# Kernel optimization log

Hardware: AMD Instinct MI355X
Metric: run time of the kernel (lower is better)

Reference implementation:

```python
import jax, jax.numpy as jnp
import numpy as np

N_CON = 100000
NUM_VAR = 100000
E = 1250000
H = 64


def setup_inputs() -> dict:
    key = jax.random.key(0)
    ks = jax.random.split(key, 6)
    x_con = jax.random.normal(ks[0], (N_CON, H), dtype=jnp.float32)
    src = jax.random.randint(ks[1], (E,), 0, N_CON, dtype=jnp.int32)
    dst = jax.random.randint(ks[2], (E,), 0, NUM_VAR, dtype=jnp.int32)
    W = jax.random.normal(ks[3], (H, H), dtype=jnp.float32) * (1.0 / np.sqrt(H))
    b = jax.random.normal(ks[4], (H,), dtype=jnp.float32) * 0.02
    gamma = jnp.ones((H,), dtype=jnp.float32)
    beta = jnp.zeros((H,), dtype=jnp.float32)
    return {"x_con": x_con, "src": src, "dst": dst, "num_var": NUM_VAR,
            "W": W, "b": b, "gamma": gamma, "beta": beta}


def reference(x_con, src, dst, num_var, W, b, gamma, beta):
    # gather -> linear: (E, H)
    msg = x_con[src] @ W.T + b
    # degree (bincount) and degree-normalized scatter-add
    deg = jnp.zeros((num_var,), dtype=msg.dtype).at[dst].add(1.0)
    agg = jnp.zeros((num_var, msg.shape[1]), dtype=msg.dtype).at[dst].add(msg)
    agg = agg / (deg[:, None] + 1e-6)
    h = jax.nn.relu(agg)
    # LayerNorm (eps=1e-5, affine)
    mu = jnp.mean(h, axis=-1, keepdims=True)
    var = jnp.mean((h - mu) ** 2, axis=-1, keepdims=True)
    return (h - mu) * jax.lax.rsqrt(var + 1e-5) * gamma + beta
```

## Files before the change

kernel.cpp:

```cpp
#include <hip/hip_runtime.h>
#include <math.h>

#define HDIM 64
#define VPB 64
#define NBR 1600
#define MAXCAP 1072
#define PKSHIFT 25
#define PKMASK 0x1FFFFFF
#define SSTR 36

typedef __attribute__((ext_vector_type(8))) short s8v;
typedef __attribute__((ext_vector_type(4))) float f4v;

__device__ __forceinline__ int pkbf(float lo, float hi) {
    unsigned ul = __float_as_uint(lo) + 0x8000u;
    unsigned uh = __float_as_uint(hi) + 0x8000u;
    return (int)((ul >> 16) | (uh & 0xffff0000u));
}

__global__ __launch_bounds__(1024) void k_partition(
        const int* __restrict__ src, const int* __restrict__ dst,
        int* __restrict__ pairs, int* __restrict__ bcur,
        int E, int NB, int CAP) {
    __shared__ int hist[NBR], cur[NBR], gb[NBR];
    int t = threadIdx.x;
    int e0 = blockIdx.x << 12;

    for (int j = t; j < NBR; j += 1024) { hist[j] = 0; cur[j] = 0; }
    __syncthreads();

    int pk[4], bb[4];
    #pragma unroll
    for (int k = 0; k < 4; ++k) {
        int e = e0 + (k << 10) + t;
        pk[k] = -1; bb[k] = 0;
        if (e < E) {
            int d = dst[e];
            bb[k] = d >> 6;
            pk[k] = ((d & (VPB - 1)) << PKSHIFT) | src[e];
            atomicAdd(&hist[bb[k]], 1);
        }
    }
    __syncthreads();
    for (int j = t; j < NB; j += 1024) {
        int h = hist[j];
        if (h) gb[j] = j * CAP + atomicAdd(&bcur[j << 4], h);
    }
    __syncthreads();
    #pragma unroll
    for (int k = 0; k < 4; ++k) {
        if (pk[k] != -1) {
            int b = bb[k];
            int r = atomicAdd(&cur[b], 1);
            int g = gb[b] + r;
            if (g < (b + 1) * CAP) pairs[g] = pk[k];
        }
    }
}

__global__ __launch_bounds__(256, 4) void k_fused(
        const float* __restrict__ x, const int* __restrict__ pairs,
        const int* __restrict__ bcur, const float* __restrict__ W,
        const float* __restrict__ b, const float* __restrict__ gamma,
        const float* __restrict__ beta, float* __restrict__ out,
        int V, int CAP) {
    __shared__ int pbuf[MAXCAP];
    __shared__ int sidx[MAXCAP];
    __shared__ int vcnt[VPB], vcur[VPB], voff[VPB];
    __shared__ int sums[4 * 16 * SSTR];
    int t = threadIdx.x;
    int blk = blockIdx.x;
    int base = blk * CAP;
    int cnt = bcur[blk << 4]; if (cnt > CAP) cnt = CAP;

    if (t < VPB) vcnt[t] = 0;
    __syncthreads();
    for (int e = t; e < cnt; e += 256) {
        int pk = pairs[base + e];
        pbuf[e] = pk;
        atomicAdd(&vcnt[((unsigned)pk) >> PKSHIFT], 1);
    }
    __syncthreads();
    if (t < 64) {
        int c0 = vcnt[t];
        int pre = c0;
        #pragma unroll
        for (int off = 1; off < 64; off <<= 1) {
            int u = __shfl_up(pre, off, 64);
            if (t >= off) pre += u;
        }
        voff[t] = pre - c0;
        vcur[t] = pre - c0;
    }
    __syncthreads();
    for (int e = t; e < cnt; e += 256) {
        int pk = pbuf[e];
        int slot = atomicAdd(&vcur[((unsigned)pk) >> PKSHIFT], 1);
        sidx[slot] = pk & PKMASK;
    }
    __syncthreads();

    int wv = t >> 6, lane = t & 63, q = lane >> 4, c = lane & 15;
    int sbase = wv * (16 * SSTR);

    for (int j = 0; j < 8; ++j) {
        int lv0 = j << 1, lv1 = lv0 + 1;
        int vl0 = (wv << 4) + lv0, vl1 = vl0 + 1;
        int start0 = voff[vl0], dg0 = vcnt[vl0];
        int start1 = voff[vl1], dg1 = vcnt[vl1];

        float a0x = 0, a0y = 0, a0z = 0, a0w = 0;
        float a1x = 0, a1y = 0, a1z = 0, a1w = 0;
        int n = dg0 > dg1 ? dg0 : dg1;
        for (int t0 = 0; t0 < n; t0 += 16) {
            #pragma unroll
            for (int k = 0; k < 4; ++k) {
                int ii = t0 + (k << 2) + q;
                if (ii < dg0) {
                    int s = sidx[start0 + ii];
                    const float4 xv = *(const float4*)(x + ((size_t)s << 6) + (c << 2));
                    a0x += xv.x; a0y += xv.y; a0z += xv.z; a0w += xv.w;
                }
                if (ii < dg1) {
                    int s = sidx[start1 + ii];
                    const float4 xv = *(const float4*)(x + ((size_t)s << 6) + (c << 2));
                    a1x += xv.x; a1y += xv.y; a1z += xv.z; a1w += xv.w;
                }
            }
        }
        a0x += __shfl_xor(a0x, 16, 64); a1x += __shfl_xor(a1x, 16, 64);
        a0y += __shfl_xor(a0y, 16, 64); a1y += __shfl_xor(a1y, 16, 64);
        a0z += __shfl_xor(a0z, 16, 64); a1z += __shfl_xor(a1z, 16, 64);
        a0w += __shfl_xor(a0w, 16, 64); a1w += __shfl_xor(a1w, 16, 64);
        a0x += __shfl_xor(a0x, 32, 64); a1x += __shfl_xor(a1x, 32, 64);
        a0y += __shfl_xor(a0y, 32, 64); a1y += __shfl_xor(a1y, 32, 64);
        a0z += __shfl_xor(a0z, 32, 64); a1z += __shfl_xor(a1z, 32, 64);
        a0w += __shfl_xor(a0w, 32, 64); a1w += __shfl_xor(a1w, 32, 64);

        if (q == 0) {
            int o0 = sbase + lv0 * SSTR + (c << 1);
            sums[o0]     = pkbf(a0x, a0y);
            sums[o0 + 1] = pkbf(a0z, a0w);
            int o1 = sbase + lv1 * SSTR + (c << 1);
            sums[o1]     = pkbf(a1x, a1y);
            sums[o1 + 1] = pkbf(a1z, a1w);
        }
    }
    __builtin_amdgcn_wave_barrier();

    union { int i4[4]; s8v v; } af[4][2];
    #pragma unroll
    for (int i = 0; i < 4; ++i)
        #pragma unroll
        for (int hh = 0; hh < 2; ++hh) {
            const float* wp = W + (((i << 4) + c) << 6) + (hh << 5) + (q << 3);
            float4 wa = *(const float4*)wp;
            float4 wb = *(const float4*)(wp + 4);
            af[i][hh].i4[0] = pkbf(wa.x, wa.y);
            af[i][hh].i4[1] = pkbf(wa.z, wa.w);
            af[i][hh].i4[2] = pkbf(wb.x, wb.y);
            af[i][hh].i4[3] = pkbf(wb.z, wb.w);
        }
    int so = sbase + c * SSTR + (q << 2);
    union { int4 i; s8v v; } bf1, bf2;
    bf1.i = *(const int4*)&sums[so];
    bf2.i = *(const int4*)&sums[so + 16];

    f4v acc[4];
    #pragma unroll
    for (int i = 0; i < 4; ++i) {
        acc[i] = (f4v){0.f, 0.f, 0.f, 0.f};
        acc[i] = __builtin_amdgcn_mfma_f32_16x16x32_bf16(af[i][0].v, bf1.v, acc[i], 0, 0, 0);
        acc[i] = __builtin_amdgcn_mfma_f32_16x16x32_bf16(af[i][1].v, bf2.v, acc[i], 0, 0, 0);
    }

    float dv  = (float)vcnt[(wv << 4) + c];
    float inv = 1.0f / (dv + 1e-6f);
    float tb  = dv * inv;
    float hreg[16];
    float s1 = 0.f, s2 = 0.f;
    #pragma unroll
    for (int i = 0; i < 4; ++i) {
        float4 bv = *(const float4*)(b + (i << 4) + (q << 2));
        float hv;
        hv = fmaxf(fmaf(bv.x, tb, acc[i][0] * inv), 0.f); hreg[(i<<2)+0] = hv; s1 += hv; s2 = fmaf(hv, hv, s2);
        hv = fmaxf(fmaf(bv.y, tb, acc[i][1] * inv), 0.f); hreg[(i<<2)+1] = hv; s1 += hv; s2 = fmaf(hv, hv, s2);
        hv = fmaxf(fmaf(bv.z, tb, acc[i][2] * inv), 0.f); hreg[(i<<2)+2] = hv; s1 += hv; s2 = fmaf(hv, hv, s2);
        hv = fmaxf(fmaf(bv.w, tb, acc[i][3] * inv), 0.f); hreg[(i<<2)+3] = hv; s1 += hv; s2 = fmaf(hv, hv, s2);
    }
    s1 += __shfl_xor(s1, 16, 64); s1 += __shfl_xor(s1, 32, 64);
    s2 += __shfl_xor(s2, 16, 64); s2 += __shfl_xor(s2, 32, 64);
    float mu   = s1 * (1.0f / 64.0f);
    float var  = fmaxf(s2 * (1.0f / 64.0f) - mu * mu, 0.0f);
    float rstd = rsqrtf(var + 1e-5f);
    float c0n  = -mu * rstd;

    int v = blk * VPB + (wv << 4) + c;
    if (v < V) {
        #pragma unroll
        for (int i = 0; i < 4; ++i) {
            float4 gv  = *(const float4*)(gamma + (i << 4) + (q << 2));
            float4 btv = *(const float4*)(beta  + (i << 4) + (q << 2));
            float4 o;
            o.x = fmaf(fmaf(hreg[(i<<2)+0], rstd, c0n), gv.x, btv.x);
            o.y = fmaf(fmaf(hreg[(i<<2)+1], rstd, c0n), gv.y, btv.y);
            o.z = fmaf(fmaf(hreg[(i<<2)+2], rstd, c0n), gv.z, btv.z);
            o.w = fmaf(fmaf(hreg[(i<<2)+3], rstd, c0n), gv.w, btv.w);
            *(float4*)(out + ((size_t)v << 6) + (i << 4) + (q << 2)) = o;
        }
    }
}

extern "C" void kernel_launch(void* const* d_in, const int* in_sizes, int n_in,
                              void* d_out, int out_size, void* d_ws, size_t ws_size,
                              hipStream_t stream) {
    const float* x_con = (const float*)d_in[0];
    const int*   src   = (const int*)d_in[1];
    const int*   dst   = (const int*)d_in[2];
    const float* W     = (const float*)d_in[4];
    const float* b     = (const float*)d_in[5];
    const float* gamma = (const float*)d_in[6];
    const float* beta  = (const float*)d_in[7];
    float* out = (float*)d_out;

    int E = in_sizes[1];
    int V = out_size / HDIM;

    int NB = (V + VPB - 1) / VPB;
    int avg = (E + NB - 1) / NB;
    int CAP = avg + (avg >> 3) + 160;
    CAP = (CAP + 15) & ~15;
    if (CAP > MAXCAP) CAP = MAXCAP;

    int* pairs = (int*)d_ws;
    int* bcur  = pairs + (size_t)NB * CAP;

    hipMemsetAsync(bcur, 0, (size_t)NB * 16 * sizeof(int), stream);
    k_partition<<<(E + 4095) / 4096, 1024, 0, stream>>>(src, dst, pairs, bcur, E, NB, CAP);
    k_fused<<<NB, 256, 0, stream>>>(x_con, pairs, bcur, W, b, gamma, beta, out, V, CAP);
}
```

Before: 173.4 us.

## Gather bf16 copy of node features built during partition, four vertices per pass

```diff
diff --git a/kernel.cpp b/kernel.cpp
--- a/kernel.cpp
+++ b/kernel.cpp
@@ -17,11 +17,14 @@
     unsigned uh = __float_as_uint(hi) + 0x8000u;
     return (int)((ul >> 16) | (uh & 0xffff0000u));
 }
+__device__ __forceinline__ float bflo(unsigned u) { return __uint_as_float(u << 16); }
+__device__ __forceinline__ float bfhi(unsigned u) { return __uint_as_float(u & 0xffff0000u); }
 
 __global__ __launch_bounds__(1024) void k_partition(
         const int* __restrict__ src, const int* __restrict__ dst,
-        int* __restrict__ pairs, int* __restrict__ bcur,
-        int E, int NB, int CAP) {
+        const float* __restrict__ x, int* __restrict__ pairs,
+        int* __restrict__ bcur, unsigned* __restrict__ xb,
+        int E, int NB, int CAP, int NXP) {
     __shared__ int hist[NBR], cur[NBR], gb[NBR];
     int t = threadIdx.x;
     int e0 = blockIdx.x << 12;
@@ -56,10 +59,14 @@
             if (g < (b + 1) * CAP) pairs[g] = pk[k];
         }
     }
+    for (int i = blockIdx.x * 1024 + t; i < NXP; i += gridDim.x * 1024) {
+        float2 xv = ((const float2*)x)[i];
+        xb[i] = (unsigned)pkbf(xv.x, xv.y);
+    }
 }
 
 __global__ __launch_bounds__(256, 4) void k_fused(
-        const float* __restrict__ x, const int* __restrict__ pairs,
+        const unsigned* __restrict__ xb, const int* __restrict__ pairs,
         const int* __restrict__ bcur, const float* __restrict__ W,
         const float* __restrict__ b, const float* __restrict__ gamma,
         const float* __restrict__ beta, float* __restrict__ out,
@@ -100,54 +107,60 @@
     }
     __syncthreads();
 
-    int wv = t >> 6, lane = t & 63, q = lane >> 4, c = lane & 15;
+    int wv = t >> 6, lane = t & 63;
+    int o = lane >> 3, u = lane & 7;
     int sbase = wv * (16 * SSTR);
 
-    for (int j = 0; j < 8; ++j) {
-        int lv0 = j << 1, lv1 = lv0 + 1;
-        int vl0 = (wv << 4) + lv0, vl1 = vl0 + 1;
-        int start0 = voff[vl0], dg0 = vcnt[vl0];
-        int start1 = voff[vl1], dg1 = vcnt[vl1];
-
-        float a0x = 0, a0y = 0, a0z = 0, a0w = 0;
-        float a1x = 0, a1y = 0, a1z = 0, a1w = 0;
-        int n = dg0 > dg1 ? dg0 : dg1;
-        for (int t0 = 0; t0 < n; t0 += 16) {
+    for (int g = 0; g < 4; ++g) {
+        int vbase = (wv << 4) + (g << 2);
+        int st[4], dg[4];
+        #pragma unroll
+        for (int m = 0; m < 4; ++m) { st[m] = voff[vbase + m]; dg[m] = vcnt[vbase + m]; }
+        float acc[4][8];
+        #pragma unroll
+        for (int m = 0; m < 4; ++m)
             #pragma unroll
-            for (int k = 0; k < 4; ++k) {
-                int ii = t0 + (k << 2) + q;
-                if (ii < dg0) {
-                    int s = sidx[start0 + ii];
-                    const float4 xv = *(const float4*)(x + ((size_t)s << 6) + (c << 2));
-                    a0x += xv.x; a0y += xv.y; a0z += xv.z; a0w += xv.w;
-                }
-                if (ii < dg1) {
-                    int s = sidx[start1 + ii];
-                    const float4 xv = *(const float4*)(x + ((size_t)s << 6) + (c << 2));
-                    a1x += xv.x; a1y += xv.y; a1z += xv.z; a1w += xv.w;
+            for (int k = 0; k < 8; ++k) acc[m][k] = 0.f;
+        int n01 = dg[0] > dg[1] ? dg[0] : dg[1];
+        int n23 = dg[2] > dg[3] ? dg[2] : dg[3];
+        int nmax = n01 > n23 ? n01 : n23;
+        for (int t0 = 0; t0 < nmax; t0 += 8) {
+            int ii = t0 + o;
+            #pragma unroll
+            for (int m = 0; m < 4; ++m) {
+                if (ii < dg[m]) {
+                    int s = sidx[st[m] + ii];
+                    uint4 xv = *(const uint4*)(xb + ((size_t)s << 5) + (u << 2));
+                    acc[m][0] += bflo(xv.x); acc[m][1] += bfhi(xv.x);
+                    acc[m][2] += bflo(xv.y); acc[m][3] += bfhi(xv.y);
+                    acc[m][4] += bflo(xv.z); acc[m][5] += bfhi(xv.z);
+                    acc[m][6] += bflo(xv.w); acc[m][7] += bfhi(xv.w);
                 }
             }
         }
-        a0x += __shfl_xor(a0x, 16, 64); a1x += __shfl_xor(a1x, 16, 64);
-        a0y += __shfl_xor(a0y, 16, 64); a1y += __shfl_xor(a1y, 16, 64);
-        a0z += __shfl_xor(a0z, 16, 64); a1z += __shfl_xor(a1z, 16, 64);
-        a0w += __shfl_xor(a0w, 16, 64); a1w += __shfl_xor(a1w, 16, 64);
-        a0x += __shfl_xor(a0x, 32, 64); a1x += __shfl_xor(a1x, 32, 64);
-        a0y += __shfl_xor(a0y, 32, 64); a1y += __shfl_xor(a1y, 32, 64);
-        a0z += __shfl_xor(a0z, 32, 64); a1z += __shfl_xor(a1z, 32, 64);
-        a0w += __shfl_xor(a0w, 32, 64); a1w += __shfl_xor(a1w, 32, 64);
-
-        if (q == 0) {
-            int o0 = sbase + lv0 * SSTR + (c << 1);
-            sums[o0]     = pkbf(a0x, a0y);
-            sums[o0 + 1] = pkbf(a0z, a0w);
-            int o1 = sbase + lv1 * SSTR + (c << 1);
-            sums[o1]     = pkbf(a1x, a1y);
-            sums[o1 + 1] = pkbf(a1z, a1w);
+        #pragma unroll
+        for (int m = 0; m < 4; ++m) {
+            #pragma unroll
+            for (int k = 0; k < 8; ++k) {
+                float v = acc[m][k];
+                v += __shfl_xor(v, 8, 64);
+                v += __shfl_xor(v, 16, 64);
+                v += __shfl_xor(v, 32, 64);
+                acc[m][k] = v;
+            }
+            if (o == m) {
+                int lv = (g << 2) + m;
+                int soff = sbase + lv * SSTR + (u << 2);
+                sums[soff + 0] = pkbf(acc[m][0], acc[m][1]);
+                sums[soff + 1] = pkbf(acc[m][2], acc[m][3]);
+                sums[soff + 2] = pkbf(acc[m][4], acc[m][5]);
+                sums[soff + 3] = pkbf(acc[m][6], acc[m][7]);
+            }
         }
     }
     __builtin_amdgcn_wave_barrier();
 
+    int q = lane >> 4, c = lane & 15;
     union { int i4[4]; s8v v; } af[4][2];
     #pragma unroll
     for (int i = 0; i < 4; ++i)
@@ -201,12 +214,12 @@
         for (int i = 0; i < 4; ++i) {
             float4 gv  = *(const float4*)(gamma + (i << 4) + (q << 2));
             float4 btv = *(const float4*)(beta  + (i << 4) + (q << 2));
-            float4 o;
-            o.x = fmaf(fmaf(hreg[(i<<2)+0], rstd, c0n), gv.x, btv.x);
-            o.y = fmaf(fmaf(hreg[(i<<2)+1], rstd, c0n), gv.y, btv.y);
-            o.z = fmaf(fmaf(hreg[(i<<2)+2], rstd, c0n), gv.z, btv.z);
-            o.w = fmaf(fmaf(hreg[(i<<2)+3], rstd, c0n), gv.w, btv.w);
-            *(float4*)(out + ((size_t)v << 6) + (i << 4) + (q << 2)) = o;
+            float4 oo;
+            oo.x = fmaf(fmaf(hreg[(i<<2)+0], rstd, c0n), gv.x, btv.x);
+            oo.y = fmaf(fmaf(hreg[(i<<2)+1], rstd, c0n), gv.y, btv.y);
+            oo.z = fmaf(fmaf(hreg[(i<<2)+2], rstd, c0n), gv.z, btv.z);
+            oo.w = fmaf(fmaf(hreg[(i<<2)+3], rstd, c0n), gv.w, btv.w);
+            *(float4*)(out + ((size_t)v << 6) + (i << 4) + (q << 2)) = oo;
         }
     }
 }
@@ -225,6 +238,7 @@
 
     int E = in_sizes[1];
     int V = out_size / HDIM;
+    int NXP = in_sizes[0] >> 1;
 
     int NB = (V + VPB - 1) / VPB;
     int avg = (E + NB - 1) / NB;
@@ -232,10 +246,12 @@
     CAP = (CAP + 15) & ~15;
     if (CAP > MAXCAP) CAP = MAXCAP;
 
-    int* pairs = (int*)d_ws;
-    int* bcur  = pairs + (size_t)NB * CAP;
+    int* pairs    = (int*)d_ws;
+    int* bcur     = pairs + (size_t)NB * CAP;
+    unsigned* xb  = (unsigned*)(bcur + (size_t)NB * 16);
 
     hipMemsetAsync(bcur, 0, (size_t)NB * 16 * sizeof(int), stream);
-    k_partition<<<(E + 4095) / 4096, 1024, 0, stream>>>(src, dst, pairs, bcur, E, NB, CAP);
-    k_fused<<<NB, 256, 0, stream>>>(x_con, pairs, bcur, W, b, gamma, beta, out, V, CAP);
-}
+    k_partition<<<(E + 4095) / 4096, 1024, 0, stream>>>(src, dst, x_con, pairs,
+                                                        bcur, xb, E, NB, CAP, NXP);
+    k_fused<<<NB, 256, 0, stream>>>(xb, pairs, bcur, W, b, gamma, beta, out, V, CAP);
+}
```

After: 176.3 us. About the same (+1.6%).
